# Performance work log

Measured on AMD Instinct MI355X. Metric: run time of the kernel, lower is better.

The kernel has to match this reference:

```python
import jax, jax.numpy as jnp
import numpy as np

B, S, D, H, R, P = 4, 8192, 512, 8, 64, 4
HD = D // H  # 64
EPS = 1e-6


def _sketch_p4(z, G1, G2):
    # sketchwithnegativity(z, 2): M1 = M2 = z
    inv_sqrt_r = 1.0 / np.sqrt(R).astype(np.float32)
    half = inv_sqrt_r * ((z @ G1) * (z @ G2))  # [B,H,S,R]
    return half * half  # sketch(): half * half for p=4


def setup_inputs() -> dict:
    key = jax.random.key(0)
    ks = jax.random.split(key, 16)
    lin = lambda k: jax.random.normal(k, (D, D), jnp.float32) * (1.0 / np.sqrt(D))
    g = lambda k: jax.random.normal(k, (HD, R), jnp.float32) * (1.0 / np.sqrt(R))
    return {
        "x": jax.random.normal(ks[0], (B, S, D), jnp.float32),
        "Wq": lin(ks[1]), "bq": jnp.zeros((D,), jnp.float32),
        "Wk": lin(ks[2]), "bk": jnp.zeros((D,), jnp.float32),
        "Wv": lin(ks[3]), "bv": jnp.zeros((D,), jnp.float32),
        "Wp": lin(ks[4]), "bp": jnp.zeros((D,), jnp.float32),
        "gamma_q": jnp.ones((1,), jnp.float32), "beta_q": jnp.zeros((1,), jnp.float32),
        "gamma_k": jnp.ones((1,), jnp.float32), "beta_k": jnp.zeros((1,), jnp.float32),
        "qG1": g(ks[5]), "qG2": g(ks[6]),
        "kG1": g(ks[7]), "kG2": g(ks[8]),
    }


def reference(x, Wq, bq, Wk, bk, Wv, bv, Wp, bp,
              gamma_q, beta_q, gamma_k, beta_k, qG1, qG2, kG1, kG2):
    b, s, d = x.shape
    split = lambda t: t.reshape(b, s, H, HD).transpose(0, 2, 1, 3)  # [B,H,S,HD]
    q = split(x @ Wq + bq)
    k = split(x @ Wk + bk)
    v = split(x @ Wv + bv)
    q = gamma_q * q + beta_q
    k = gamma_k * k + beta_k
    phi_q = _sketch_p4(q, qG1, qG2)  # [B,H,S,R]
    phi_k = _sketch_p4(k, kG1, kG2)  # [B,H,S,R]
    # linear-attention form of attn = (phi_q phi_k^T) / rowsum; avoids [S,S]
    kv = jnp.einsum('bhsr,bhsd->bhrd', phi_k, v)          # [B,H,R,HD]
    ksum = phi_k.sum(axis=2)                              # [B,H,R]
    num = jnp.einsum('bhqr,bhrd->bhqd', phi_q, kv)        # [B,H,S,HD]
    den = jnp.einsum('bhqr,bhr->bhq', phi_q, ksum) + EPS  # [B,H,S]
    out = num / den[..., None]
    out = out.transpose(0, 2, 1, 3).reshape(b, s, d)
    return out @ Wp + bp
```

## Files before the change

kernel.cpp:

```cpp
#include <hip/hip_runtime.h>
#include <hip/hip_bf16.h>


#define SEQ 8192

typedef __attribute__((ext_vector_type(8))) short bf16x8;
typedef __attribute__((ext_vector_type(4))) float f32x4;

__device__ __forceinline__ unsigned short f2b(float f) {
    union { float f; unsigned int i; } v; v.f = f;
    unsigned int r = v.i + 0x7fffu + ((v.i >> 16) & 1u);
    return (unsigned short)(r >> 16);
}
__device__ __forceinline__ float b2f(unsigned short u) {
    union { unsigned int i; float f; } v; v.i = ((unsigned int)u) << 16; return v.f;
}

#if __has_builtin(__builtin_amdgcn_global_load_lds)
#define ASYNC_CP 1
#endif

__device__ __forceinline__ void cp16(const unsigned short* g, unsigned short* l) {
#ifdef ASYNC_CP
    __builtin_amdgcn_global_load_lds(
        (const __attribute__((address_space(1))) unsigned int*)g,
        (__attribute__((address_space(3))) unsigned int*)l, 16, 0, 0);
#endif
}

__global__ __launch_bounds__(256) void prep_all(
    const float* __restrict__ x, unsigned short* __restrict__ xb,
    const float* __restrict__ Wv, const float* __restrict__ Wp,
    unsigned short* __restrict__ WTf, unsigned short* __restrict__ WTp,
    const float* __restrict__ Wq, const float* __restrict__ bq,
    const float* __restrict__ Wk, const float* __restrict__ bk,
    const float* __restrict__ bv,
    const float* __restrict__ gq, const float* __restrict__ bbq,
    const float* __restrict__ gk, const float* __restrict__ bbk,
    const float* __restrict__ qG1, const float* __restrict__ qG2,
    const float* __restrict__ kG1, const float* __restrict__ kG2,
    float* __restrict__ cvec)
{
    const int blk = blockIdx.x;
    const int tid = threadIdx.x;

    if (blk < 8192) {
        size_t i = ((size_t)blk * 256 + tid) * 8;
        float4 a = *(const float4*)&x[i];
        float4 b = *(const float4*)&x[i + 4];
        ushort4 o1 = { f2b(a.x), f2b(a.y), f2b(a.z), f2b(a.w) };
        ushort4 o2 = { f2b(b.x), f2b(b.y), f2b(b.z), f2b(b.w) };
        *(ushort4*)&xb[i]     = o1;
        *(ushort4*)&xb[i + 4] = o2;
        return;
    }

    if (blk < 8704) {
        const int idx = blk - 8192;
        const int z = idx >> 8;
        const float* W = (z == 0) ? Wv : Wp;
        unsigned short* O = (z == 0) ? (WTf + (size_t)2048 * 512) : WTp;
        __shared__ float t[32][33];
        const int tx = tid & 31, ty = tid >> 5;
        const int k0 = ((idx >> 4) & 15) * 32, n0 = (idx & 15) * 32;
        #pragma unroll
        for (int i = 0; i < 4; ++i)
            t[ty + 8 * i][tx] = W[(size_t)(k0 + ty + 8 * i) * 512 + n0 + tx];
        __syncthreads();
        #pragma unroll
        for (int i = 0; i < 4; ++i)
            O[(size_t)(n0 + ty + 8 * i) * 512 + k0 + tx] = f2b(t[tx][ty + 8 * i]);
        return;
    }

    const int idx = blk - 8704;
    if (idx == 512) {
        for (int i = tid; i < 512; i += 256) cvec[2048 + i] = bv[i];
        return;
    }
    const int bi = idx & 31, ky = idx >> 5;
    const int zz = bi >> 4, h = (bi >> 1) & 7, p = bi & 1;
    const float* W    = zz ? Wk : Wq;
    const float* bias = zz ? bk : bq;
    const float* G    = zz ? (p ? kG2 : kG1) : (p ? qG2 : qG1);
    const float  gamma = zz ? gk[0] : gq[0];
    const float  beta  = zz ? bbk[0] : bbq[0];

    __shared__ float Gs[64][65];
    for (int i = tid; i < 4096; i += 256) Gs[i >> 6][i & 63] = G[i];
    __syncthreads();

    const int rr = tid & 63, kg = tid >> 6;
    const int jc = zz * 1024 + h * 128 + rr * 2 + p;
    const int k0 = ky * 32;
    for (int k = k0 + kg; k < k0 + 32; k += 4) {
        float s = 0.f;
        const float* wrow = &W[(size_t)k * 512 + h * 64];
        #pragma unroll 8
        for (int j = 0; j < 64; ++j) s = fmaf(wrow[j], Gs[j][rr], s);
        WTf[(size_t)jc * 512 + k] = f2b(gamma * s);
    }
    if (kg == 0 && ky == 0) {
        float cb = 0.f, cg = 0.f;
        #pragma unroll 8
        for (int j = 0; j < 64; ++j) {
            cb = fmaf(bias[h * 64 + j], Gs[j][rr], cb);
            cg += Gs[j][rr];
        }
        cvec[jc] = gamma * cb + beta * cg;
    }
}

__global__ __launch_bounds__(256) void gemm_mfma_fused(
    const unsigned short* __restrict__ xb,
    const unsigned short* __restrict__ WTf,
    const float* __restrict__ cvec,
    unsigned short* __restrict__ PHIQ, unsigned short* __restrict__ PHIKT,
    unsigned short* __restrict__ VT)
{
    __shared__ __align__(16) unsigned short As[128 * 32];
    __shared__ __align__(16) unsigned short Bs[128 * 32];

    const int tid = threadIdx.x;
    const int w = tid >> 6, lane = tid & 63;
    const int flat = blockIdx.x;
    const int xcd = flat & 7, slot = flat >> 3;
    const int n0 = (xcd * 32 + slot / 20) * 128;
    const int j0 = (slot % 20) * 128;
    const int wr = w >> 1, wc = w & 1;

    const int r0 = w * 32 + (lane >> 2);
    const int kq = (lane & 3) * 8;
    const unsigned short* gA = &xb[(size_t)(n0 + r0) * 512 + kq];
    const unsigned short* gB = &WTf[(size_t)(j0 + r0) * 512 + kq];
    unsigned short* lA = &As[(w * 32) * 32];
    unsigned short* lB = &Bs[(w * 32) * 32];

    f32x4 acc[4][4];
    #pragma unroll
    for (int i = 0; i < 4; ++i)
        #pragma unroll
        for (int j = 0; j < 4; ++j) { acc[i][j] = (f32x4){0.f, 0.f, 0.f, 0.f}; }

    const int cr = (lane >> 4) * 8;

    for (int k0 = 0; k0 < 512; k0 += 32) {
        __syncthreads();
#ifdef ASYNC_CP
        cp16(gA + k0, lA);
        cp16(gA + 16 * 512 + k0, lA + 16 * 32);
        cp16(gB + k0, lB);
        cp16(gB + 16 * 512 + k0, lB + 16 * 32);
#else
        { uint4 v = *(const uint4*)(gA + k0);            *(uint4*)(lA + (size_t)lane * 8) = v; }
        { uint4 v = *(const uint4*)(gA + 16 * 512 + k0); *(uint4*)(lA + 16 * 32 + (size_t)lane * 8) = v; }
        { uint4 v = *(const uint4*)(gB + k0);            *(uint4*)(lB + (size_t)lane * 8) = v; }
        { uint4 v = *(const uint4*)(gB + 16 * 512 + k0); *(uint4*)(lB + 16 * 32 + (size_t)lane * 8) = v; }
#endif
        __syncthreads();

        bf16x8 af[4], bfr[4];
        #pragma unroll
        for (int i = 0; i < 4; ++i) {
            af[i]  = *(const bf16x8*)&As[(wr * 64 + i * 16 + (lane & 15)) * 32 + cr];
            bfr[i] = *(const bf16x8*)&Bs[(wc * 64 + i * 16 + (lane & 15)) * 32 + cr];
        }
        #pragma unroll
        for (int mi = 0; mi < 4; ++mi)
            #pragma unroll
            for (int ni = 0; ni < 4; ++ni)
                acc[mi][ni] = __builtin_amdgcn_mfma_f32_16x16x32_bf16(
                    af[mi], bfr[ni], acc[mi][ni], 0, 0, 0);
    }

    const int bq = n0 >> 13;
    const int sq = n0 & (SEQ - 1);
    const int t0 = sq + wr * 64 + (lane >> 4) * 4;

    if (j0 < 2048) {
        const int zq = j0 >> 10;
        const int h  = (j0 >> 7) & 7;
        #pragma unroll
        for (int ni = 0; ni < 4; ++ni) {
            const int loc = wc * 64 + ni * 16 + (lane & 15);
            const float cv = cvec[j0 + loc];
            const int rr = loc >> 1;
            #pragma unroll
            for (int mi = 0; mi < 4; ++mi) {
                float ph[4];
                #pragma unroll
                for (int r = 0; r < 4; ++r) {
                    float u = acc[mi][ni][r] + cv;
                    float up = __shfl_xor(u, 1);
                    float hh = 0.125f * u * up;
                    ph[r] = hh * hh;
                }
                if ((lane & 1) == 0) {
                    if (zq == 0) {
                        #pragma unroll
                        for (int r = 0; r < 4; ++r)
                            PHIQ[((size_t)(bq * 8 + h) * SEQ + t0 + mi * 16 + r) * 64 + rr]
                                = f2b(ph[r]);
                    } else {
                        ushort4 o = { f2b(ph[0]), f2b(ph[1]), f2b(ph[2]), f2b(ph[3]) };
                        *(ushort4*)&PHIKT[((size_t)((bq * 8 + h) * 64 + rr)) * SEQ
                                          + t0 + mi * 16] = o;
                    }
                }
            }
        }
    } else {
        #pragma unroll
        for (int ni = 0; ni < 4; ++ni) {
            const int loc = wc * 64 + ni * 16 + (lane & 15);
            const int n = (j0 - 2048) + loc;
            const float cv = cvec[j0 + loc];
            #pragma unroll
            for (int mi = 0; mi < 4; ++mi) {
                ushort4 o = { f2b(acc[mi][ni][0] + cv), f2b(acc[mi][ni][1] + cv),
                              f2b(acc[mi][ni][2] + cv), f2b(acc[mi][ni][3] + cv) };
                *(ushort4*)&VT[((size_t)(bq * 512 + n)) * SEQ + t0 + mi * 16] = o;
            }
        }
    }
}

__global__ __launch_bounds__(256) void gemm_mfma_final(
    const unsigned short* __restrict__ Ab,
    const unsigned short* __restrict__ WTp,
    const float* __restrict__ bias, float* __restrict__ out)
{
    __shared__ __align__(16) unsigned short As[128 * 32];
    __shared__ __align__(16) unsigned short Bs[128 * 32];

    const int tid = threadIdx.x;
    const int w = tid >> 6, lane = tid & 63;
    const int flat = blockIdx.x;
    const int xcd = flat & 7, slot = flat >> 3;
    const int n0 = (xcd * 32 + (slot >> 2)) * 128;
    const int j0 = (slot & 3) * 128;
    const int wr = w >> 1, wc = w & 1;

    const int r0 = w * 32 + (lane >> 2);
    const int kq = (lane & 3) * 8;
    const unsigned short* gA = &Ab[(size_t)(n0 + r0) * 512 + kq];
    const unsigned short* gB = &WTp[(size_t)(j0 + r0) * 512 + kq];
    unsigned short* lA = &As[(w * 32) * 32];
    unsigned short* lB = &Bs[(w * 32) * 32];

    f32x4 acc[4][4];
    #pragma unroll
    for (int i = 0; i < 4; ++i)
        #pragma unroll
        for (int j = 0; j < 4; ++j) { acc[i][j] = (f32x4){0.f, 0.f, 0.f, 0.f}; }

    const int cr = (lane >> 4) * 8;

    for (int k0 = 0; k0 < 512; k0 += 32) {
        __syncthreads();
#ifdef ASYNC_CP
        cp16(gA + k0, lA);
        cp16(gA + 16 * 512 + k0, lA + 16 * 32);
        cp16(gB + k0, lB);
        cp16(gB + 16 * 512 + k0, lB + 16 * 32);
#else
        { uint4 v = *(const uint4*)(gA + k0);            *(uint4*)(lA + (size_t)lane * 8) = v; }
        { uint4 v = *(const uint4*)(gA + 16 * 512 + k0); *(uint4*)(lA + 16 * 32 + (size_t)lane * 8) = v; }
        { uint4 v = *(const uint4*)(gB + k0);            *(uint4*)(lB + (size_t)lane * 8) = v; }
        { uint4 v = *(const uint4*)(gB + 16 * 512 + k0); *(uint4*)(lB + 16 * 32 + (size_t)lane * 8) = v; }
#endif
        __syncthreads();

        bf16x8 af[4], bfr[4];
        #pragma unroll
        for (int i = 0; i < 4; ++i) {
            af[i]  = *(const bf16x8*)&As[(wr * 64 + i * 16 + (lane & 15)) * 32 + cr];
            bfr[i] = *(const bf16x8*)&Bs[(wc * 64 + i * 16 + (lane & 15)) * 32 + cr];
        }
        #pragma unroll
        for (int mi = 0; mi < 4; ++mi)
            #pragma unroll
            for (int ni = 0; ni < 4; ++ni)
                acc[mi][ni] = __builtin_amdgcn_mfma_f32_16x16x32_bf16(
                    af[mi], bfr[ni], acc[mi][ni], 0, 0, 0);
    }

    #pragma unroll
    for (int ni = 0; ni < 4; ++ni) {
        const int jcol = j0 + wc * 64 + ni * 16 + (lane & 15);
        const float bvv = bias[jcol];
        #pragma unroll
        for (int mi = 0; mi < 4; ++mi) {
            #pragma unroll
            for (int r = 0; r < 4; ++r) {
                const int t = n0 + wr * 64 + mi * 16 + (lane >> 4) * 4 + r;
                out[(size_t)t * 512 + jcol] = acc[mi][ni][r] + bvv;
            }
        }
    }
}

__global__ __launch_bounds__(256) void kv_mfma(
    const unsigned short* __restrict__ PHIKT, const unsigned short* __restrict__ VT,
    float* __restrict__ KVP, float* __restrict__ KSP)
{
    const int bh = blockIdx.x, seg = blockIdx.y;
    const int tid = threadIdx.x;
    const int w = tid >> 6, lane = tid & 63;
    const size_t pbase =
        ((size_t)bh * 64 + w * 16 + (lane & 15)) * SEQ + seg * 512 + (lane >> 4) * 8;
    const size_t vbase =
        ((size_t)((bh >> 3) * 512 + (bh & 7) * 64 + (lane & 15))) * SEQ
        + seg * 512 + (lane >> 4) * 8;

    f32x4 acc[4], ks;
    #pragma unroll
    for (int nt = 0; nt < 4; ++nt) acc[nt] = (f32x4){0.f, 0.f, 0.f, 0.f};
    ks = (f32x4){0.f, 0.f, 0.f, 0.f};
    bf16x8 ones;
    #pragma unroll
    for (int i = 0; i < 8; ++i) ones[i] = (short)0x3f80;

    #pragma unroll 2
    for (int k = 0; k < 512; k += 32) {
        bf16x8 a = *(const bf16x8*)&PHIKT[pbase + k];
        ks = __builtin_amdgcn_mfma_f32_16x16x32_bf16(a, ones, ks, 0, 0, 0);
        #pragma unroll
        for (int nt = 0; nt < 4; ++nt) {
            bf16x8 bb = *(const bf16x8*)&VT[vbase + (size_t)nt * 16 * SEQ + k];
            acc[nt] = __builtin_amdgcn_mfma_f32_16x16x32_bf16(a, bb, acc[nt], 0, 0, 0);
        }
    }

    float* kvp = &KVP[((size_t)bh * 16 + seg) * 4096];
    #pragma unroll
    for (int nt = 0; nt < 4; ++nt) {
        float4 o = { acc[nt][0], acc[nt][1], acc[nt][2], acc[nt][3] };
        *(float4*)&kvp[(nt * 16 + (lane & 15)) * 64 + w * 16 + (lane >> 4) * 4] = o;
    }
    if ((lane & 15) == 0) {
        float4 o = { ks[0], ks[1], ks[2], ks[3] };
        *(float4*)&KSP[((size_t)bh * 16 + seg) * 64 + w * 16 + (lane >> 4) * 4] = o;
    }
}

__global__ __launch_bounds__(256) void kv_reduce(
    const float* __restrict__ KVP, const float* __restrict__ KSP,
    float* __restrict__ KV, float* __restrict__ KS)
{
    const int bh = blockIdx.x;
    const int e0 = blockIdx.y * 512;
    for (int e = e0 + threadIdx.x; e < e0 + 512; e += 256) {
        float s = 0.f;
        #pragma unroll 8
        for (int c = 0; c < 16; ++c) s += KVP[(size_t)(bh * 16 + c) * 4096 + e];
        KV[(size_t)bh * 4096 + e] = s;
    }
    if (blockIdx.y == 0 && threadIdx.x < 64) {
        float s = 0.f;
        for (int c = 0; c < 16; ++c) s += KSP[(bh * 16 + c) * 64 + threadIdx.x];
        KS[bh * 64 + threadIdx.x] = s;
    }
}

__global__ __launch_bounds__(256) void attn_mfma(
    const unsigned short* __restrict__ PHIQ, const float* __restrict__ KV,
    const float* __restrict__ KS, unsigned short* __restrict__ OAb)
{
    __shared__ __align__(16) unsigned short bpad[144 * 72];
    const int bh = blockIdx.x, st = blockIdx.y;
    const int tid = threadIdx.x;
    const int b = bh >> 3, h = bh & 7;

    for (int i = tid; i < 144 * 64; i += 256) {
        const int n = i >> 6, r = i & 63;
        float val;
        if (n < 64)        val = KV[(size_t)bh * 4096 + n * 64 + r];
        else if (n < 128)  { float x = KV[(size_t)bh * 4096 + (n - 64) * 64 + r];
                             val = x - b2f(f2b(x)); }
        else if (n == 128) val = KS[bh * 64 + r];
        else if (n == 129) { float x = KS[bh * 64 + r]; val = x - b2f(f2b(x)); }
        else               val = 0.f;
        bpad[n * 72 + r] = f2b(val);
    }
    __syncthreads();

    const int w = tid >> 6, lane = tid & 63;
    bf16x8 bf[9][2];
    #pragma unroll
    for (int nt = 0; nt < 9; ++nt) {
        const unsigned short* bp = &bpad[(nt * 16 + (lane & 15)) * 72 + (lane >> 4) * 8];
        bf[nt][0] = *(const bf16x8*)bp;
        bf[nt][1] = *(const bf16x8*)(bp + 32);
    }

    const int tw = st * 256 + w * 64;
    #pragma unroll
    for (int mt = 0; mt < 4; ++mt) {
        const unsigned short* ap =
            &PHIQ[((size_t)bh * SEQ + tw + mt * 16 + (lane & 15)) * 64 + (lane >> 4) * 8];
        bf16x8 a0 = *(const bf16x8*)ap;
        bf16x8 a1 = *(const bf16x8*)(ap + 32);
        f32x4 acc[9];
        #pragma unroll
        for (int nt = 0; nt < 9; ++nt) acc[nt] = (f32x4){0.f, 0.f, 0.f, 0.f};
        #pragma unroll
        for (int nt = 0; nt < 9; ++nt) {
            acc[nt] = __builtin_amdgcn_mfma_f32_16x16x32_bf16(a0, bf[nt][0], acc[nt], 0, 0, 0);
            acc[nt] = __builtin_amdgcn_mfma_f32_16x16x32_bf16(a1, bf[nt][1], acc[nt], 0, 0, 0);
        }
        #pragma unroll
        for (int r4 = 0; r4 < 4; ++r4) {
            const float den = __shfl(acc[8][r4], (lane & 48)) +
                              __shfl(acc[8][r4], (lane & 48) + 1) + 1e-6f;
            const float inv = 1.0f / den;
            const int s = tw + mt * 16 + (lane >> 4) * 4 + r4;
            #pragma unroll
            for (int nt = 0; nt < 4; ++nt)
                OAb[((size_t)b * SEQ + s) * 512 + h * 64 + nt * 16 + (lane & 15)] =
                    f2b((acc[nt][r4] + acc[nt + 4][r4]) * inv);
        }
    }
}

extern "C" void kernel_launch(void* const* d_in, const int* in_sizes, int n_in,
                              void* d_out, int out_size, void* d_ws, size_t ws_size,
                              hipStream_t stream)
{
    (void)in_sizes; (void)n_in; (void)out_size; (void)ws_size;
    const float* x   = (const float*)d_in[0];
    const float* Wq  = (const float*)d_in[1];
    const float* bq  = (const float*)d_in[2];
    const float* Wk  = (const float*)d_in[3];
    const float* bk  = (const float*)d_in[4];
    const float* Wv  = (const float*)d_in[5];
    const float* bv  = (const float*)d_in[6];
    const float* Wp  = (const float*)d_in[7];
    const float* bp  = (const float*)d_in[8];
    const float* gq  = (const float*)d_in[9];
    const float* bbq = (const float*)d_in[10];
    const float* gk  = (const float*)d_in[11];
    const float* bbk = (const float*)d_in[12];
    const float* qG1 = (const float*)d_in[13];
    const float* qG2 = (const float*)d_in[14];
    const float* kG1 = (const float*)d_in[15];
    const float* kG2 = (const float*)d_in[16];

    unsigned short* PHIQ  = (unsigned short*)d_ws;
    unsigned short* PHIKT = PHIQ + 16777216;
    unsigned short* VT    = PHIKT + 16777216;
    unsigned short* xb    = VT   + 16777216;
    unsigned short* OAb   = xb   + 16777216;
    unsigned short* WTf   = OAb  + 16777216;
    unsigned short* WTp   = WTf  + 2560 * 512;
    float* cvec = (float*)(WTp + 262144);
    float* KVP  = cvec + 2560;
    float* KSP  = KVP + 4194304;
    float* KV   = KSP + 65536;
    float* KS   = KV + 131072;
    float* out  = (float*)d_out;

    hipLaunchKernelGGL(prep_all, dim3(9217), dim3(256), 0, stream,
                       x, xb, Wv, Wp, WTf, WTp,
                       Wq, bq, Wk, bk, bv, gq, bbq, gk, bbk,
                       qG1, qG2, kG1, kG2, cvec);
    hipLaunchKernelGGL(gemm_mfma_fused, dim3(5120), dim3(256), 0, stream,
                       xb, WTf, cvec, PHIQ, PHIKT, VT);
    hipLaunchKernelGGL(kv_mfma, dim3(32, 16), dim3(256), 0, stream,
                       PHIKT, VT, KVP, KSP);
    hipLaunchKernelGGL(kv_reduce, dim3(32, 8), dim3(256), 0, stream, KVP, KSP, KV, KS);
    hipLaunchKernelGGL(attn_mfma, dim3(32, 32), dim3(256), 0, stream,
                       PHIQ, KV, KS, OAb);
    hipLaunchKernelGGL(gemm_mfma_final, dim3(1024), dim3(256), 0, stream,
                       OAb, WTp, bp, out);
}
```

Before: 409.0 us.

## Double-buffer LDS tiles in MFMA GEMMs and split KV reduction finer

Both MFMA GEMM kernels now keep two LDS tile buffers and issue the async global-to-LDS copy of the next K tile while computing on the current one. This hides load latency and removes one barrier per K step. Separately, kv_mfma splits the sequence into 32 segments instead of 16 for more parallelism, so kv_reduce now sums twice as many partials. The cost is doubled LDS per block, which may reduce occupancy, plus more partial-sum traffic. The KVP buffer has to hold 32 partials per head where it used to hold 16.

```diff
diff --git a/kernel.cpp b/kernel.cpp
--- a/kernel.cpp
+++ b/kernel.cpp
@@ -111,6 +111,30 @@
     }
 }
 
+#define STAGE_T(kk, dA, dB)                                                     \
+    do {                                                                        \
+        cp16(gA + (kk), dA);                                                    \
+        cp16(gA + 16 * 512 + (kk), dA + 16 * 32);                               \
+        cp16(gB + (kk), dB);                                                    \
+        cp16(gB + 16 * 512 + (kk), dB + 16 * 32);                               \
+    } while (0)
+
+#define COMPUTE_T(SA, SB)                                                       \
+    do {                                                                        \
+        bf16x8 af[4], bfr[4];                                                   \
+        _Pragma("unroll")                                                       \
+        for (int i = 0; i < 4; ++i) {                                           \
+            af[i]  = *(const bf16x8*)&(SA)[(wr * 64 + i * 16 + (lane & 15)) * 32 + cr]; \
+            bfr[i] = *(const bf16x8*)&(SB)[(wc * 64 + i * 16 + (lane & 15)) * 32 + cr]; \
+        }                                                                       \
+        _Pragma("unroll")                                                       \
+        for (int mi = 0; mi < 4; ++mi)                                          \
+            _Pragma("unroll")                                                   \
+            for (int ni = 0; ni < 4; ++ni)                                      \
+                acc[mi][ni] = __builtin_amdgcn_mfma_f32_16x16x32_bf16(          \
+                    af[mi], bfr[ni], acc[mi][ni], 0, 0, 0);                     \
+    } while (0)
+
 __global__ __launch_bounds__(256) void gemm_mfma_fused(
     const unsigned short* __restrict__ xb,
     const unsigned short* __restrict__ WTf,
@@ -118,8 +142,8 @@
     unsigned short* __restrict__ PHIQ, unsigned short* __restrict__ PHIKT,
     unsigned short* __restrict__ VT)
 {
-    __shared__ __align__(16) unsigned short As[128 * 32];
-    __shared__ __align__(16) unsigned short Bs[128 * 32];
+    __shared__ __align__(16) unsigned short As[2][128 * 32];
+    __shared__ __align__(16) unsigned short Bs[2][128 * 32];
 
     const int tid = threadIdx.x;
     const int w = tid >> 6, lane = tid & 63;
@@ -133,8 +157,10 @@
     const int kq = (lane & 3) * 8;
     const unsigned short* gA = &xb[(size_t)(n0 + r0) * 512 + kq];
     const unsigned short* gB = &WTf[(size_t)(j0 + r0) * 512 + kq];
-    unsigned short* lA = &As[(w * 32) * 32];
-    unsigned short* lB = &Bs[(w * 32) * 32];
+    unsigned short* lA0 = &As[0][(w * 32) * 32];
+    unsigned short* lA1 = &As[1][(w * 32) * 32];
+    unsigned short* lB0 = &Bs[0][(w * 32) * 32];
+    unsigned short* lB1 = &Bs[1][(w * 32) * 32];
 
     f32x4 acc[4][4];
     #pragma unroll
@@ -144,33 +170,17 @@
 
     const int cr = (lane >> 4) * 8;
 
-    for (int k0 = 0; k0 < 512; k0 += 32) {
+    STAGE_T(0, lA0, lB0);
+    __syncthreads();
+
+    #pragma unroll 1
+    for (int tt = 0; tt < 16; tt += 2) {
+        STAGE_T((tt + 1) * 32, lA1, lB1);
+        COMPUTE_T(As[0], Bs[0]);
         __syncthreads();
-#ifdef ASYNC_CP
-        cp16(gA + k0, lA);
-        cp16(gA + 16 * 512 + k0, lA + 16 * 32);
-        cp16(gB + k0, lB);
-        cp16(gB + 16 * 512 + k0, lB + 16 * 32);
-#else
-        { uint4 v = *(const uint4*)(gA + k0);            *(uint4*)(lA + (size_t)lane * 8) = v; }
-        { uint4 v = *(const uint4*)(gA + 16 * 512 + k0); *(uint4*)(lA + 16 * 32 + (size_t)lane * 8) = v; }
-        { uint4 v = *(const uint4*)(gB + k0);            *(uint4*)(lB + (size_t)lane * 8) = v; }
-        { uint4 v = *(const uint4*)(gB + 16 * 512 + k0); *(uint4*)(lB + 16 * 32 + (size_t)lane * 8) = v; }
-#endif
+        if (tt + 2 < 16) STAGE_T((tt + 2) * 32, lA0, lB0);
+        COMPUTE_T(As[1], Bs[1]);
         __syncthreads();
-
-        bf16x8 af[4], bfr[4];
-        #pragma unroll
-        for (int i = 0; i < 4; ++i) {
-            af[i]  = *(const bf16x8*)&As[(wr * 64 + i * 16 + (lane & 15)) * 32 + cr];
-            bfr[i] = *(const bf16x8*)&Bs[(wc * 64 + i * 16 + (lane & 15)) * 32 + cr];
-        }
-        #pragma unroll
-        for (int mi = 0; mi < 4; ++mi)
-            #pragma unroll
-            for (int ni = 0; ni < 4; ++ni)
-                acc[mi][ni] = __builtin_amdgcn_mfma_f32_16x16x32_bf16(
-                    af[mi], bfr[ni], acc[mi][ni], 0, 0, 0);
     }
 
     const int bq = n0 >> 13;
@@ -230,8 +240,8 @@
     const unsigned short* __restrict__ WTp,
     const float* __restrict__ bias, float* __restrict__ out)
 {
-    __shared__ __align__(16) unsigned short As[128 * 32];
-    __shared__ __align__(16) unsigned short Bs[128 * 32];
+    __shared__ __align__(16) unsigned short As[2][128 * 32];
+    __shared__ __align__(16) unsigned short Bs[2][128 * 32];
 
     const int tid = threadIdx.x;
     const int w = tid >> 6, lane = tid & 63;
@@ -245,8 +255,10 @@
     const int kq = (lane & 3) * 8;
     const unsigned short* gA = &Ab[(size_t)(n0 + r0) * 512 + kq];
     const unsigned short* gB = &WTp[(size_t)(j0 + r0) * 512 + kq];
-    unsigned short* lA = &As[(w * 32) * 32];
-    unsigned short* lB = &Bs[(w * 32) * 32];
+    unsigned short* lA0 = &As[0][(w * 32) * 32];
+    unsigned short* lA1 = &As[1][(w * 32) * 32];
+    unsigned short* lB0 = &Bs[0][(w * 32) * 32];
+    unsigned short* lB1 = &Bs[1][(w * 32) * 32];
 
     f32x4 acc[4][4];
     #pragma unroll
@@ -256,33 +268,17 @@
 
     const int cr = (lane >> 4) * 8;
 
-    for (int k0 = 0; k0 < 512; k0 += 32) {
+    STAGE_T(0, lA0, lB0);
+    __syncthreads();
+
+    #pragma unroll 1
+    for (int tt = 0; tt < 16; tt += 2) {
+        STAGE_T((tt + 1) * 32, lA1, lB1);
+        COMPUTE_T(As[0], Bs[0]);
         __syncthreads();
-#ifdef ASYNC_CP
-        cp16(gA + k0, lA);
-        cp16(gA + 16 * 512 + k0, lA + 16 * 32);
-        cp16(gB + k0, lB);
-        cp16(gB + 16 * 512 + k0, lB + 16 * 32);
-#else
-        { uint4 v = *(const uint4*)(gA + k0);            *(uint4*)(lA + (size_t)lane * 8) = v; }
-        { uint4 v = *(const uint4*)(gA + 16 * 512 + k0); *(uint4*)(lA + 16 * 32 + (size_t)lane * 8) = v; }
-        { uint4 v = *(const uint4*)(gB + k0);            *(uint4*)(lB + (size_t)lane * 8) = v; }
-        { uint4 v = *(const uint4*)(gB + 16 * 512 + k0); *(uint4*)(lB + 16 * 32 + (size_t)lane * 8) = v; }
-#endif
+        if (tt + 2 < 16) STAGE_T((tt + 2) * 32, lA0, lB0);
+        COMPUTE_T(As[1], Bs[1]);
         __syncthreads();
-
-        bf16x8 af[4], bfr[4];
-        #pragma unroll
-        for (int i = 0; i < 4; ++i) {
-            af[i]  = *(const bf16x8*)&As[(wr * 64 + i * 16 + (lane & 15)) * 32 + cr];
-            bfr[i] = *(const bf16x8*)&Bs[(wc * 64 + i * 16 + (lane & 15)) * 32 + cr];
-        }
-        #pragma unroll
-        for (int mi = 0; mi < 4; ++mi)
-            #pragma unroll
-            for (int ni = 0; ni < 4; ++ni)
-                acc[mi][ni] = __builtin_amdgcn_mfma_f32_16x16x32_bf16(
-                    af[mi], bfr[ni], acc[mi][ni], 0, 0, 0);
     }
 
     #pragma unroll
@@ -308,10 +304,10 @@
     const int tid = threadIdx.x;
     const int w = tid >> 6, lane = tid & 63;
     const size_t pbase =
-        ((size_t)bh * 64 + w * 16 + (lane & 15)) * SEQ + seg * 512 + (lane >> 4) * 8;
+        ((size_t)bh * 64 + w * 16 + (lane & 15)) * SEQ + seg * 256 + (lane >> 4) * 8;
     const size_t vbase =
         ((size_t)((bh >> 3) * 512 + (bh & 7) * 64 + (lane & 15))) * SEQ
-        + seg * 512 + (lane >> 4) * 8;
+        + seg * 256 + (lane >> 4) * 8;
 
     f32x4 acc[4], ks;
     #pragma unroll
@@ -322,7 +318,7 @@
     for (int i = 0; i < 8; ++i) ones[i] = (short)0x3f80;
 
     #pragma unroll 2
-    for (int k = 0; k < 512; k += 32) {
+    for (int k = 0; k < 256; k += 32) {
         bf16x8 a = *(const bf16x8*)&PHIKT[pbase + k];
         ks = __builtin_amdgcn_mfma_f32_16x16x32_bf16(a, ones, ks, 0, 0, 0);
         #pragma unroll
@@ -332,7 +328,7 @@
         }
     }
 
-    float* kvp = &KVP[((size_t)bh * 16 + seg) * 4096];
+    float* kvp = &KVP[((size_t)bh * 32 + seg) * 4096];
     #pragma unroll
     for (int nt = 0; nt < 4; ++nt) {
         float4 o = { acc[nt][0], acc[nt][1], acc[nt][2], acc[nt][3] };
@@ -340,7 +336,7 @@
     }
     if ((lane & 15) == 0) {
         float4 o = { ks[0], ks[1], ks[2], ks[3] };
-        *(float4*)&KSP[((size_t)bh * 16 + seg) * 64 + w * 16 + (lane >> 4) * 4] = o;
+        *(float4*)&KSP[((size_t)bh * 32 + seg) * 64 + w * 16 + (lane >> 4) * 4] = o;
     }
 }
 
@@ -353,12 +349,12 @@
     for (int e = e0 + threadIdx.x; e < e0 + 512; e += 256) {
         float s = 0.f;
         #pragma unroll 8
-        for (int c = 0; c < 16; ++c) s += KVP[(size_t)(bh * 16 + c) * 4096 + e];
+        for (int c = 0; c < 32; ++c) s += KVP[(size_t)(bh * 32 + c) * 4096 + e];
         KV[(size_t)bh * 4096 + e] = s;
     }
     if (blockIdx.y == 0 && threadIdx.x < 64) {
         float s = 0.f;
-        for (int c = 0; c < 16; ++c) s += KSP[(bh * 16 + c) * 64 + threadIdx.x];
+        for (int c = 0; c < 32; ++c) s += KSP[(bh * 32 + c) * 64 + threadIdx.x];
         KS[bh * 64 + threadIdx.x] = s;
     }
 }
@@ -466,7 +462,7 @@
                        qG1, qG2, kG1, kG2, cvec);
     hipLaunchKernelGGL(gemm_mfma_fused, dim3(5120), dim3(256), 0, stream,
                        xb, WTf, cvec, PHIQ, PHIKT, VT);
-    hipLaunchKernelGGL(kv_mfma, dim3(32, 16), dim3(256), 0, stream,
+    hipLaunchKernelGGL(kv_mfma, dim3(32, 32), dim3(256), 0, stream,
                        PHIKT, VT, KVP, KSP);
     hipLaunchKernelGGL(kv_reduce, dim3(32, 8), dim3(256), 0, stream, KVP, KSP, KV, KS);
     hipLaunchKernelGGL(attn_mfma, dim3(32, 32), dim3(256), 0, stream,
```

New measurement: 425.9 us. 1.04x slower.
